# Kernel optimization log

Measured on AMD Instinct MI355X. Metric: run time of the kernel, lower is better.

Reference implementation:

```python
import jax, jax.numpy as jnp
import numpy as np

B, C, NMAX = 256, 1, 256   # graphs, channels, max nodes per graph
N = B * C * NMAX           # total nodes = 65536
E = N * 16                 # edges = 1,048,576
EMB, HID = 128, 128


def setup_inputs() -> dict:
    key = jax.random.key(0)
    ks = jax.random.split(key, 8)
    adj = jax.random.uniform(ks[0], (B, C, NMAX, NMAX), jnp.float32)
    edges = jax.random.randint(ks[1], (E, 2), 0, N, dtype=jnp.int32)
    subgraph_idx = jnp.repeat(jnp.arange(B, dtype=jnp.int32), C * NMAX)
    def lin(k, fan_in, fan_out):
        return jax.random.normal(k, (fan_in, fan_out), jnp.float32) / np.sqrt(fan_in).astype(np.float32)
    return {
        "adj": adj, "edges": edges, "subgraph_idx": subgraph_idx,
        "Wdec": lin(ks[2], NMAX, EMB), "bdec": jnp.zeros((EMB,), jnp.float32),
        "Wc1": lin(ks[3], EMB, HID),   "bc1": jnp.zeros((HID,), jnp.float32),
        "Wc2": lin(ks[4], HID, HID),   "bc2": jnp.zeros((HID,), jnp.float32),
        "Wp1": lin(ks[5], HID, HID),   "bp1": jnp.zeros((HID,), jnp.float32),
        "Wp2": lin(ks[6], HID, 1),     "bp2": jnp.zeros((1,), jnp.float32),
    }


def gcn_conv(x, W, b, src, dst):
    # PyG GCNConv: h = x W; add self-loops; symmetric normalization D^-1/2 (A+I) D^-1/2; + bias
    h = x @ W                                      # [N, out]
    deg = jnp.zeros((N,), x.dtype).at[dst].add(1.0) + 1.0  # in-degree incl. self loop
    dinv = jax.lax.rsqrt(deg)                      # [N]
    coef = dinv[src] * dinv[dst]                   # [E]
    agg = jax.ops.segment_sum(h[src] * coef[:, None], dst, num_segments=N)
    return agg + h * (dinv * dinv)[:, None] + b    # self-loop term + bias


def reference(adj, edges, subgraph_idx, Wdec, bdec, Wc1, bc1, Wc2, bc2, Wp1, bp1, Wp2, bp2):
    src, dst = edges[:, 0], edges[:, 1]
    # decoder_input: Linear(max_num_nodes -> embedding_dim) on flattened adjacency rows
    x = adj.reshape(-1, NMAX) @ Wdec + bdec        # [N, EMB]
    # forward applies convs[:-1] only (2 of the 3 convs); dropout is identity in eval mode
    x = jax.nn.relu(gcn_conv(x, Wc1, bc1, src, dst))
    x = jax.nn.relu(gcn_conv(x, Wc2, bc2, src, dst))
    # global max pool over nodes of each graph
    pooled = jax.ops.segment_max(x, subgraph_idx, num_segments=B)  # [B, HID]
    # post_mp MLP head
    h = jax.nn.relu(pooled @ Wp1 + bp1)
    return h @ Wp2 + bp2                           # [B, 1]
```

## Files before the change

### kernel.cpp

```cpp
#include <hip/hip_runtime.h>
#include <hip/hip_fp16.h>
#include <cstdint>
#include <cstddef>

#define NN   65536
#define NE   1048576
#define FD   128
#define KDEC 256
#define NGRAPH 256
#define NEP_MAX (NE + 15 * NN)
#define DUMMY_SRC 65536u
#define EPB  4096
#define BCAP 4608

typedef __attribute__((ext_vector_type(8))) short s16x8;
typedef __attribute__((ext_vector_type(4))) float f32x4;

__device__ __forceinline__ ushort f2bf(float x) {
  uint u = __float_as_uint(x);
  uint r = (u + 0x7fffu + ((u >> 16) & 1u)) >> 16;
  return (ushort)r;
}
__device__ __forceinline__ float bf2f(ushort h) {
  return __uint_as_float(((uint)h) << 16);
}


__global__ __launch_bounds__(1024) void k_histbin(const int* __restrict__ edges,
                                                  uint* __restrict__ ec,
                                                  uint* __restrict__ binbuf,
                                                  int* __restrict__ gbin) {
  const int b = blockIdx.x, t = threadIdx.x;
  if (b >= 256) {
    int fi = (b - 256) * 4096 + t * 4;
    *(uint4*)(ec + fi) = make_uint4(DUMMY_SRC, DUMMY_SRC, DUMMY_SRC, DUMMY_SRC);
    return;
  }
  __shared__ int lcnt[256];
  __shared__ int lsum[256];
  __shared__ int gbase[256];
  __shared__ uint sorted[EPB];

  if (t < 256) lcnt[t] = 0;
  __syncthreads();

  uint rec[4];
  ushort bkt[4], lidx[4];
#pragma unroll
  for (int r = 0; r < 4; r++) {
    int i = b * EPB + r * 1024 + t;
    int2 e = ((const int2*)edges)[i];
    int bucket = e.y >> 8;
    int li = atomicAdd(&lcnt[bucket], 1);
    rec[r] = ((uint)bucket << 24) | ((uint)(e.y & 255) << 16) | (uint)e.x;
    bkt[r] = (ushort)bucket;
    lidx[r] = (ushort)li;
  }
  __syncthreads();

  if (t < 256) lsum[t] = lcnt[t];
  __syncthreads();
  for (int off = 1; off < 256; off <<= 1) {
    int v = 0;
    if (t < 256 && t >= off) v = lsum[t - off];
    __syncthreads();
    if (t < 256) lsum[t] += v;
    __syncthreads();
  }
  if (t < 256) gbase[t] = atomicAdd(&gbin[t], lcnt[t]);
  __syncthreads();

#pragma unroll
  for (int r = 0; r < 4; r++) {
    int B = bkt[r];
    sorted[lsum[B] - lcnt[B] + lidx[r]] = rec[r];
  }
  __syncthreads();

  for (int s = t; s < EPB; s += 1024) {
    uint v = sorted[s];
    int B = v >> 24;
    int ex = lsum[B] - lcnt[B];
    binbuf[B * BCAP + gbase[B] + (s - ex)] = v & 0xFFFFFFu;
  }
}

__global__ __launch_bounds__(256) void k_bscatter(const uint* __restrict__ binbuf,
                                                  const int* __restrict__ gbin,
                                                  const int* __restrict__ offs,
                                                  uint* __restrict__ ec) {
  __shared__ int cnt2[256];
  int b = blockIdx.x, t = threadIdx.x;
  cnt2[t] = 0;
  __syncthreads();
  int m = gbin[b];
  int nb = b << 8;
  for (int i = t; i < m; i += 256) {
    uint rec = binbuf[b * BCAP + i];
    int dlow = rec >> 16;
    int pos = offs[nb + dlow] + atomicAdd(&cnt2[dlow], 1);
    ec[pos] = rec & 0xFFFFu;
  }
}

__device__ __forceinline__ void prep_one(const float* __restrict__ W,
                                         ushort* __restrict__ H,
                                         ushort* __restrict__ L, int i) {
  int k = i >> 7, c = i & 127;
  float w = W[i];
  ushort h = f2bf(w);
  ushort lo = f2bf(w - bf2f(h));
  size_t dst = ((size_t)((k >> 5) * 8 + (c >> 4)) * 64 +
                (size_t)((c & 15) + 16 * ((k & 31) >> 3))) * 8 + (k & 7);
  H[dst] = h;
  L[dst] = lo;
}

__global__ __launch_bounds__(256) void k_misc1(const uint* __restrict__ binbuf,
                                               const int* __restrict__ gbin,
                                               int* __restrict__ hist,
                                               int* __restrict__ bsum,
                                               const float* __restrict__ Wdec,
                                               const float* __restrict__ Wc1,
                                               const float* __restrict__ bdec,
                                               float* __restrict__ wfused,
                                               float* __restrict__ bfused,
                                               const float* __restrict__ Wc2,
                                               ushort* __restrict__ w2h,
                                               ushort* __restrict__ w2l) {
  int b = blockIdx.x, t = threadIdx.x;
  if (b < 256) {
    __shared__ int lc[256];
    __shared__ int s[256];
    lc[t] = 0;
    __syncthreads();
    int m = gbin[b];
    for (int i = t; i < m; i += 256)
      atomicAdd(&lc[binbuf[b * BCAP + i] >> 16], 1);
    __syncthreads();
    hist[b * 256 + t] = lc[t];
    s[t] = (lc[t] + 15) & ~15;
    __syncthreads();
    for (int st = 128; st > 0; st >>= 1) {
      if (t < st) s[t] += s[t + st];
      __syncthreads();
    }
    if (t == 0) bsum[b] = s[0];
  } else if (b < 384) {
    int i = (b - 256) * 256 + t;
    int k = i >> 7, c = i & 127;
    float acc = 0.f;
#pragma unroll 8
    for (int j = 0; j < 128; j++) acc = fmaf(Wdec[k * FD + j], Wc1[j * FD + c], acc);
    wfused[i] = acc;
    if (b == 256 && t < 128) {
      float ba = 0.f;
      for (int j = 0; j < 128; j++) ba = fmaf(bdec[j], Wc1[j * FD + t], ba);
      bfused[t] = ba;
    }
  } else {
    int i = (b - 384) * 256 + t;
    prep_one(Wc2, w2h, w2l, i);
  }
}

__global__ __launch_bounds__(256) void k_misc2(const int* __restrict__ hist,
                                               const int* __restrict__ bsum,
                                               int* __restrict__ offs,
                                               float* __restrict__ dinv,
                                               const float* __restrict__ wfused,
                                               ushort* __restrict__ wfh,
                                               ushort* __restrict__ wfl) {
  int b = blockIdx.x, t = threadIdx.x;
  if (b < 256) {
    __shared__ int sb[256];
    __shared__ int s[256];
    sb[t] = bsum[t];
    int v = hist[b * 256 + t];
    int vp = (v + 15) & ~15;
    s[t] = vp;
    __syncthreads();
    for (int off = 1; off < 256; off <<= 1) {
      int addb = (t >= off) ? sb[t - off] : 0;
      int add = (t >= off) ? s[t - off] : 0;
      __syncthreads();
      sb[t] += addb;
      s[t] += add;
      __syncthreads();
    }
    int pb = (b > 0) ? sb[b - 1] : 0;
    offs[b * 256 + t] = pb + s[t] - vp;
    dinv[b * 256 + t] = rsqrtf((float)(v + 1));
  } else {
    int i = (b - 256) * 256 + t;
    prep_one(wfused, wfh, wfl, i);
  }
}


template <bool ASPLIT>
__global__ __launch_bounds__(256) void k_gemm(const void* __restrict__ A0,
                                              const void* __restrict__ A1,
                                              const ushort* __restrict__ Whi,
                                              const ushort* __restrict__ Wlo,
                                              const float* __restrict__ bias,
                                              const float* __restrict__ scale,
                                              ushort* __restrict__ Y, int K) {
  const int t = threadIdx.x;
  const int w = t >> 6;
  const int l = t & 63;
  const int lr = l & 15;
  const int kg = l >> 4;
  const int r0 = blockIdx.x * 64 + w * 16;

  f32x4 acc[8];
#pragma unroll
  for (int nb = 0; nb < 8; nb++) acc[nb] = (f32x4)0.f;

  for (int ks = 0; ks < K; ks += 32) {
    s16x8 ah, al;
    if (ASPLIT) {
      size_t base = (size_t)(r0 + lr) * K + ks + kg * 8;
      ah = *(const s16x8*)((const ushort*)A0 + base);
      al = *(const s16x8*)((const ushort*)A1 + base);
    } else {
      const float* xp = (const float*)A0 + (size_t)(r0 + lr) * K + ks + kg * 8;
      f32x4 x0 = *(const f32x4*)xp;
      f32x4 x1 = *(const f32x4*)(xp + 4);
      float xv[8] = {x0.x, x0.y, x0.z, x0.w, x1.x, x1.y, x1.z, x1.w};
      union { ushort u[8]; s16x8 v; } H, L;
#pragma unroll
      for (int e = 0; e < 8; e++) {
        ushort h = f2bf(xv[e]);
        H.u[e] = h;
        L.u[e] = f2bf(xv[e] - bf2f(h));
      }
      ah = H.v;
      al = L.v;
    }
    const size_t bbase = (size_t)(ks >> 5) * 4096 + (size_t)l * 8;
#pragma unroll
    for (int nb = 0; nb < 8; nb++) {
      s16x8 bh = *(const s16x8*)(Whi + bbase + nb * 512);
      s16x8 bl = *(const s16x8*)(Wlo + bbase + nb * 512);
      acc[nb] = __builtin_amdgcn_mfma_f32_16x16x32_bf16(ah, bh, acc[nb], 0, 0, 0);
      acc[nb] = __builtin_amdgcn_mfma_f32_16x16x32_bf16(ah, bl, acc[nb], 0, 0, 0);
      acc[nb] = __builtin_amdgcn_mfma_f32_16x16x32_bf16(al, bh, acc[nb], 0, 0, 0);
    }
  }

  float dvr[4];
#pragma unroll
  for (int r = 0; r < 4; r++)
    dvr[r] = scale ? scale[r0 + kg * 4 + r] : 1.f;

#pragma unroll
  for (int nb = 0; nb < 8; nb++) {
    int col = nb * 16 + lr;
    float bv = bias ? bias[col] : 0.f;
#pragma unroll
    for (int r = 0; r < 4; r++) {
      size_t row = (size_t)(r0 + kg * 4 + r);
      Y[row * FD + col] = f2bf((acc[nb][r] + bv) * dvr[r]);
    }
  }
}


template <int EMIT>
__global__ __launch_bounds__(256) void k_agg(const ushort* __restrict__ h16,
                                             const uint* __restrict__ ec,
                                             const int* __restrict__ offs,
                                             const int* __restrict__ hist,
                                             const float* __restrict__ dinv,
                                             const float* __restrict__ bias,
                                             ushort* __restrict__ yhi,
                                             ushort* __restrict__ ylo,
                                             float* __restrict__ pooled) {
  __shared__ int pmax[128];
  const int t = threadIdx.x;
  if (EMIT == 1) {
    if (t < 128) pmax[t] = 0;
    __syncthreads();
  }
  const int n = blockIdx.x * 4 + (t >> 6);
  const int l = t & 63;
  const int half = l >> 5;
  const int dl = (l & 31) * 4;

  const int cnt_p = (hist[n] + 15) & ~15;
  const uint* ep = ec + offs[n];

  float a0 = 0.f, a1 = 0.f, a2 = 0.f, a3 = 0.f;
  float b0 = 0.f, b1 = 0.f, b2 = 0.f, b3 = 0.f;
  for (int i = half; i < cnt_p; i += 16) {
    uint s0 = ep[i];
    uint s1 = ep[i + 2];
    uint s2 = ep[i + 4];
    uint s3 = ep[i + 6];
    uint s4 = ep[i + 8];
    uint s5 = ep[i + 10];
    uint s6 = ep[i + 12];
    uint s7 = ep[i + 14];
    ushort4 v0 = *(const ushort4*)(h16 + ((size_t)s0 << 7) + dl);
    ushort4 v1 = *(const ushort4*)(h16 + ((size_t)s1 << 7) + dl);
    ushort4 v2 = *(const ushort4*)(h16 + ((size_t)s2 << 7) + dl);
    ushort4 v3 = *(const ushort4*)(h16 + ((size_t)s3 << 7) + dl);
    ushort4 v4 = *(const ushort4*)(h16 + ((size_t)s4 << 7) + dl);
    ushort4 v5 = *(const ushort4*)(h16 + ((size_t)s5 << 7) + dl);
    ushort4 v6 = *(const ushort4*)(h16 + ((size_t)s6 << 7) + dl);
    ushort4 v7 = *(const ushort4*)(h16 + ((size_t)s7 << 7) + dl);
    a0 += bf2f(v0.x); a1 += bf2f(v0.y); a2 += bf2f(v0.z); a3 += bf2f(v0.w);
    b0 += bf2f(v1.x); b1 += bf2f(v1.y); b2 += bf2f(v1.z); b3 += bf2f(v1.w);
    a0 += bf2f(v2.x); a1 += bf2f(v2.y); a2 += bf2f(v2.z); a3 += bf2f(v2.w);
    b0 += bf2f(v3.x); b1 += bf2f(v3.y); b2 += bf2f(v3.z); b3 += bf2f(v3.w);
    a0 += bf2f(v4.x); a1 += bf2f(v4.y); a2 += bf2f(v4.z); a3 += bf2f(v4.w);
    b0 += bf2f(v5.x); b1 += bf2f(v5.y); b2 += bf2f(v5.z); b3 += bf2f(v5.w);
    a0 += bf2f(v6.x); a1 += bf2f(v6.y); a2 += bf2f(v6.z); a3 += bf2f(v6.w);
    b0 += bf2f(v7.x); b1 += bf2f(v7.y); b2 += bf2f(v7.z); b3 += bf2f(v7.w);
  }
  a0 += b0; a1 += b1; a2 += b2; a3 += b3;
  a0 += __shfl_xor(a0, 32);
  a1 += __shfl_xor(a1, 32);
  a2 += __shfl_xor(a2, 32);
  a3 += __shfl_xor(a3, 32);

  if (l < 32) {
    float dv = dinv[n];
    ushort4 vs = *(const ushort4*)(h16 + ((size_t)n << 7) + dl);
    float4 bb = *(const float4*)(bias + dl);
    float o0 = fmaxf(fmaf(dv, a0 + bf2f(vs.x), bb.x), 0.f);
    float o1 = fmaxf(fmaf(dv, a1 + bf2f(vs.y), bb.y), 0.f);
    float o2 = fmaxf(fmaf(dv, a2 + bf2f(vs.z), bb.z), 0.f);
    float o3 = fmaxf(fmaf(dv, a3 + bf2f(vs.w), bb.w), 0.f);
    if (EMIT == 0) {
      ushort4 hi, lo;
      hi.x = f2bf(o0); lo.x = f2bf(o0 - bf2f(hi.x));
      hi.y = f2bf(o1); lo.y = f2bf(o1 - bf2f(hi.y));
      hi.z = f2bf(o2); lo.z = f2bf(o2 - bf2f(hi.z));
      hi.w = f2bf(o3); lo.w = f2bf(o3 - bf2f(hi.w));
      size_t base = (size_t)n * FD + dl;
      *(ushort4*)(yhi + base) = hi;
      *(ushort4*)(ylo + base) = lo;
    } else {
      atomicMax(&pmax[dl + 0], __float_as_int(o0));
      atomicMax(&pmax[dl + 1], __float_as_int(o1));
      atomicMax(&pmax[dl + 2], __float_as_int(o2));
      atomicMax(&pmax[dl + 3], __float_as_int(o3));
    }
  }
  if (EMIT == 1) {
    __syncthreads();
    if (t < 128) {
      int gr = blockIdx.x >> 6;
      atomicMax((int*)pooled + gr * FD + t, pmax[t]);
    }
  }
}


__global__ __launch_bounds__(128) void k_mlp(const float* __restrict__ pooled,
                                             const float* __restrict__ Wp1,
                                             const float* __restrict__ bp1,
                                             const float* __restrict__ Wp2,
                                             const float* __restrict__ bp2,
                                             float* __restrict__ out) {
  __shared__ float row[128];
  __shared__ float red[128];
  int g = blockIdx.x, t = threadIdx.x;
  row[t] = pooled[g * FD + t];
  __syncthreads();
  float acc = bp1[t];
#pragma unroll 8
  for (int k = 0; k < 128; k++) acc = fmaf(row[k], Wp1[k * FD + t], acc);
  acc = fmaxf(acc, 0.f);
  red[t] = acc * Wp2[t];
  __syncthreads();
  for (int st = 64; st > 0; st >>= 1) {
    if (t < st) red[t] += red[t + st];
    __syncthreads();
  }
  if (t == 0) out[g] = red[0] + bp2[0];
}


extern "C" void kernel_launch(void* const* d_in, const int* in_sizes, int n_in,
                              void* d_out, int out_size, void* d_ws, size_t ws_size,
                              hipStream_t stream) {
  (void)in_sizes; (void)n_in; (void)out_size; (void)ws_size;

  const float* adj  = (const float*)d_in[0];
  const int*   edges= (const int*)d_in[1];
  const float* Wdec = (const float*)d_in[3];
  const float* bdec = (const float*)d_in[4];
  const float* Wc1  = (const float*)d_in[5];
  const float* bc1  = (const float*)d_in[6];
  const float* Wc2  = (const float*)d_in[7];
  const float* bc2  = (const float*)d_in[8];
  const float* Wp1  = (const float*)d_in[9];
  const float* bp1  = (const float*)d_in[10];
  const float* Wp2  = (const float*)d_in[11];
  const float* bp2  = (const float*)d_in[12];
  float* out = (float*)d_out;

  char* ws = (char*)d_ws;
  size_t off = 0;
  auto alloc = [&](size_t bytes) -> void* {
    void* p = ws + off;
    off += (bytes + 255) & ~(size_t)255;
    return p;
  };
  ushort* h16  = (ushort*)alloc((size_t)(NN + 1) * FD * 2);
  ushort* x1hi = (ushort*)alloc((size_t)NN * FD * 2);
  ushort* x1lo = (ushort*)alloc((size_t)NN * FD * 2);
  float*  pooled = (float*)alloc((size_t)NGRAPH * FD * 4);
  int*    gbin = (int*)alloc(256 * 4);
  int*    hist = (int*)alloc((size_t)NN * 4);
  int*    offs = (int*)alloc((size_t)NN * 4);
  int*    bsum = (int*)alloc(256 * 4);
  uint*   ec   = (uint*)alloc((size_t)NEP_MAX * 4);
  uint*   binbuf = (uint*)alloc((size_t)256 * BCAP * 4);
  float*  dinv = (float*)alloc((size_t)NN * 4);
  float*  wfused = (float*)alloc((size_t)KDEC * FD * 4);
  float*  bfused = (float*)alloc(FD * 4);
  ushort* wfh = (ushort*)alloc((size_t)KDEC * FD * 2);
  ushort* wfl = (ushort*)alloc((size_t)KDEC * FD * 2);
  ushort* w2h = (ushort*)alloc((size_t)FD * FD * 2);
  ushort* w2l = (ushort*)alloc((size_t)FD * FD * 2);

  hipMemsetAsync(pooled, 0, (size_t)NGRAPH * FD * 4 + 256 * 4, stream);
  hipMemsetAsync(h16 + (size_t)NN * FD, 0, FD * 2, stream);

  k_histbin<<<256 + NEP_MAX / 4096, 1024, 0, stream>>>(edges, ec, binbuf, gbin);
  k_misc1<<<448, 256, 0, stream>>>(binbuf, gbin, hist, bsum, Wdec, Wc1, bdec,
                                   wfused, bfused, Wc2, w2h, w2l);
  k_misc2<<<384, 256, 0, stream>>>(hist, bsum, offs, dinv, wfused, wfh, wfl);
  k_bscatter<<<256, 256, 0, stream>>>(binbuf, gbin, offs, ec);

  k_gemm<false><<<NN / 64, 256, 0, stream>>>(adj, nullptr, wfh, wfl, bfused, dinv, h16, KDEC);

  k_agg<0><<<NN / 4, 256, 0, stream>>>(h16, ec, offs, hist, dinv, bc1, x1hi, x1lo, nullptr);

  k_gemm<true><<<NN / 64, 256, 0, stream>>>(x1hi, x1lo, w2h, w2l, nullptr, dinv, h16, FD);

  k_agg<1><<<NN / 4, 256, 0, stream>>>(h16, ec, offs, hist, dinv, bc2, nullptr, nullptr, pooled);

  k_mlp<<<NGRAPH, 128, 0, stream>>>(pooled, Wp1, bp1, Wp2, bp2, out);
}
```

Measured before the change: 180.7 us.

## Stage GEMM weights in double-buffered LDS and compute two row tiles per wave

The GEMM kernel now cooperatively loads each 32-wide K slice of the hi/lo weight matrices into a double-buffered shared-memory tile. Each wave handles 32 rows instead of 16, so every weight fragment read from LDS feeds twice as many MFMAs. The next slice's A and B global loads are issued before the current slice's MFMAs to overlap latency. Blocks cover 128 rows, which halves the grid. The costs are more registers (16 accumulators), 32 KB of LDS per block and a barrier per K step, all of which may reduce occupancy.

```diff
diff --git a/kernel.cpp b/kernel.cpp
--- a/kernel.cpp
+++ b/kernel.cpp
@@ -206,63 +206,120 @@
                                               const float* __restrict__ bias,
                                               const float* __restrict__ scale,
                                               ushort* __restrict__ Y, int K) {
+  __shared__ ushort Bs[2][8192];
   const int t = threadIdx.x;
   const int w = t >> 6;
   const int l = t & 63;
   const int lr = l & 15;
   const int kg = l >> 4;
-  const int r0 = blockIdx.x * 64 + w * 16;
-
-  f32x4 acc[8];
-#pragma unroll
-  for (int nb = 0; nb < 8; nb++) acc[nb] = (f32x4)0.f;
-
-  for (int ks = 0; ks < K; ks += 32) {
-    s16x8 ah, al;
+  const int r0 = blockIdx.x * 128 + w * 32;
+  const int nks = K >> 5;
+
+  f32x4 acc[2][8];
+#pragma unroll
+  for (int mb = 0; mb < 2; mb++)
+#pragma unroll
+    for (int nb = 0; nb < 8; nb++) acc[mb][nb] = (f32x4)0.f;
+
+  f32x4 araw[4];
+  s16x8 ahn[2], aln[2];
+  s16x8 bh0, bh1, bl0, bl1;
+
+  auto issueA = [&](int s) {
+#pragma unroll
+    for (int mb = 0; mb < 2; mb++) {
+      size_t base = (size_t)(r0 + mb * 16 + lr) * K + s * 32 + kg * 8;
+      if (ASPLIT) {
+        ahn[mb] = *(const s16x8*)((const ushort*)A0 + base);
+        aln[mb] = *(const s16x8*)((const ushort*)A1 + base);
+      } else {
+        const float* xp = (const float*)A0 + base;
+        araw[mb * 2] = *(const f32x4*)xp;
+        araw[mb * 2 + 1] = *(const f32x4*)(xp + 4);
+      }
+    }
+  };
+  auto issueB = [&](int s) {
+    const ushort* ph = Whi + (size_t)s * 4096 + t * 16;
+    const ushort* pl = Wlo + (size_t)s * 4096 + t * 16;
+    bh0 = *(const s16x8*)ph;
+    bh1 = *(const s16x8*)(ph + 8);
+    bl0 = *(const s16x8*)pl;
+    bl1 = *(const s16x8*)(pl + 8);
+  };
+  auto writeB = [&](int buf) {
+    *(s16x8*)&Bs[buf][t * 16] = bh0;
+    *(s16x8*)&Bs[buf][t * 16 + 8] = bh1;
+    *(s16x8*)&Bs[buf][4096 + t * 16] = bl0;
+    *(s16x8*)&Bs[buf][4096 + t * 16 + 8] = bl1;
+  };
+
+  issueB(0);
+  issueA(0);
+  writeB(0);
+  __syncthreads();
+
+  int buf = 0;
+  for (int s = 0; s < nks; ++s) {
+    s16x8 ah[2], al[2];
     if (ASPLIT) {
-      size_t base = (size_t)(r0 + lr) * K + ks + kg * 8;
-      ah = *(const s16x8*)((const ushort*)A0 + base);
-      al = *(const s16x8*)((const ushort*)A1 + base);
+      ah[0] = ahn[0]; ah[1] = ahn[1];
+      al[0] = aln[0]; al[1] = aln[1];
     } else {
-      const float* xp = (const float*)A0 + (size_t)(r0 + lr) * K + ks + kg * 8;
-      f32x4 x0 = *(const f32x4*)xp;
-      f32x4 x1 = *(const f32x4*)(xp + 4);
-      float xv[8] = {x0.x, x0.y, x0.z, x0.w, x1.x, x1.y, x1.z, x1.w};
-      union { ushort u[8]; s16x8 v; } H, L;
-#pragma unroll
-      for (int e = 0; e < 8; e++) {
-        ushort h = f2bf(xv[e]);
-        H.u[e] = h;
-        L.u[e] = f2bf(xv[e] - bf2f(h));
+#pragma unroll
+      for (int mb = 0; mb < 2; mb++) {
+        float xv[8] = {araw[mb*2].x, araw[mb*2].y, araw[mb*2].z, araw[mb*2].w,
+                       araw[mb*2+1].x, araw[mb*2+1].y, araw[mb*2+1].z, araw[mb*2+1].w};
+        union { ushort u[8]; s16x8 v; } H, L;
+#pragma unroll
+        for (int e = 0; e < 8; e++) {
+          ushort h = f2bf(xv[e]);
+          H.u[e] = h;
+          L.u[e] = f2bf(xv[e] - bf2f(h));
+        }
+        ah[mb] = H.v;
+        al[mb] = L.v;
       }
-      ah = H.v;
-      al = L.v;
-    }
-    const size_t bbase = (size_t)(ks >> 5) * 4096 + (size_t)l * 8;
+    }
+    const bool more = (s + 1 < nks);
+    if (more) { issueB(s + 1); issueA(s + 1); }
+
 #pragma unroll
     for (int nb = 0; nb < 8; nb++) {
-      s16x8 bh = *(const s16x8*)(Whi + bbase + nb * 512);
-      s16x8 bl = *(const s16x8*)(Wlo + bbase + nb * 512);
-      acc[nb] = __builtin_amdgcn_mfma_f32_16x16x32_bf16(ah, bh, acc[nb], 0, 0, 0);
-      acc[nb] = __builtin_amdgcn_mfma_f32_16x16x32_bf16(ah, bl, acc[nb], 0, 0, 0);
-      acc[nb] = __builtin_amdgcn_mfma_f32_16x16x32_bf16(al, bh, acc[nb], 0, 0, 0);
-    }
-  }
-
-  float dvr[4];
-#pragma unroll
-  for (int r = 0; r < 4; r++)
-    dvr[r] = scale ? scale[r0 + kg * 4 + r] : 1.f;
+      s16x8 bh = *(const s16x8*)&Bs[buf][nb * 512 + l * 8];
+      s16x8 bl = *(const s16x8*)&Bs[buf][4096 + nb * 512 + l * 8];
+#pragma unroll
+      for (int mb = 0; mb < 2; mb++) {
+        acc[mb][nb] = __builtin_amdgcn_mfma_f32_16x16x32_bf16(ah[mb], bh, acc[mb][nb], 0, 0, 0);
+        acc[mb][nb] = __builtin_amdgcn_mfma_f32_16x16x32_bf16(ah[mb], bl, acc[mb][nb], 0, 0, 0);
+        acc[mb][nb] = __builtin_amdgcn_mfma_f32_16x16x32_bf16(al[mb], bh, acc[mb][nb], 0, 0, 0);
+      }
+    }
+    if (more) {
+      writeB(buf ^ 1);
+      __syncthreads();
+      buf ^= 1;
+    }
+  }
+
+  float dvr[2][4];
+#pragma unroll
+  for (int mb = 0; mb < 2; mb++)
+#pragma unroll
+    for (int r = 0; r < 4; r++)
+      dvr[mb][r] = scale ? scale[r0 + mb * 16 + kg * 4 + r] : 1.f;
 
 #pragma unroll
   for (int nb = 0; nb < 8; nb++) {
     int col = nb * 16 + lr;
     float bv = bias ? bias[col] : 0.f;
 #pragma unroll
-    for (int r = 0; r < 4; r++) {
-      size_t row = (size_t)(r0 + kg * 4 + r);
-      Y[row * FD + col] = f2bf((acc[nb][r] + bv) * dvr[r]);
-    }
+    for (int mb = 0; mb < 2; mb++)
+#pragma unroll
+      for (int r = 0; r < 4; r++) {
+        size_t row = (size_t)(r0 + mb * 16 + kg * 4 + r);
+        Y[row * FD + col] = f2bf((acc[mb][nb][r] + bv) * dvr[mb][r]);
+      }
   }
 }
 
@@ -437,11 +494,11 @@
   k_misc2<<<384, 256, 0, stream>>>(hist, bsum, offs, dinv, wfused, wfh, wfl);
   k_bscatter<<<256, 256, 0, stream>>>(binbuf, gbin, offs, ec);
 
-  k_gemm<false><<<NN / 64, 256, 0, stream>>>(adj, nullptr, wfh, wfl, bfused, dinv, h16, KDEC);
+  k_gemm<false><<<NN / 128, 256, 0, stream>>>(adj, nullptr, wfh, wfl, bfused, dinv, h16, KDEC);
 
   k_agg<0><<<NN / 4, 256, 0, stream>>>(h16, ec, offs, hist, dinv, bc1, x1hi, x1lo, nullptr);
 
-  k_gemm<true><<<NN / 64, 256, 0, stream>>>(x1hi, x1lo, w2h, w2l, nullptr, dinv, h16, FD);
+  k_gemm<true><<<NN / 128, 256, 0, stream>>>(x1hi, x1lo, w2h, w2l, nullptr, dinv, h16, FD);
 
   k_agg<1><<<NN / 4, 256, 0, stream>>>(h16, ec, offs, hist, dinv, bc2, nullptr, nullptr, pooled);
 
```

After: 168.3 us. 1.07x faster.
